# Kernel tuning notes

Measured on AMD Instinct MI355X. Metric: run time of the kernel, lower is better.

The kernel has to match this reference:

```python
import jax, jax.numpy as jnp
import numpy as np

N_NODES = 200000
N_EDGES = 6400000
N_GRAPHS = 2000


def _linear_params(key, fan_in, fan_out):
    k1, k2 = jax.random.split(key)
    bound = 1.0 / np.sqrt(fan_in)
    W = jax.random.uniform(k1, (fan_in, fan_out), minval=-bound, maxval=bound, dtype=jnp.float32)
    b = jax.random.uniform(k2, (fan_out,), minval=-bound, maxval=bound, dtype=jnp.float32)
    return W, b


def setup_inputs() -> dict:
    key = jax.random.key(0)
    ks = jax.random.split(key, 12)
    x = jax.random.normal(ks[0], (N_NODES, 2), dtype=jnp.float32)
    edge_index = jax.random.randint(ks[1], (2, N_EDGES), 0, N_NODES, dtype=jnp.int32)
    batch = jnp.sort(jax.random.randint(ks[2], (N_NODES,), 0, N_GRAPHS, dtype=jnp.int32))
    W1a, b1a = _linear_params(ks[3], 2, 16)
    W1b, b1b = _linear_params(ks[4], 16, 16)
    W2a, b2a = _linear_params(ks[5], 16, 16)
    W2b, b2b = _linear_params(ks[6], 16, 16)
    W3a, b3a = _linear_params(ks[7], 16, 16)
    W3b, b3b = _linear_params(ks[8], 16, 16)
    Wl1, bl1 = _linear_params(ks[9], 16, 16)
    Wl2, bl2 = _linear_params(ks[10], 16, 1)
    return dict(x=x, edge_index=edge_index, batch=batch,
                W1a=W1a, b1a=b1a, W1b=W1b, b1b=b1b,
                W2a=W2a, b2a=b2a, W2b=W2b, b2b=b2b,
                W3a=W3a, b3a=b3a, W3b=W3b, b3b=b3b,
                Wl1=Wl1, bl1=bl1, Wl2=Wl2, bl2=bl2)


def _gin_conv(x, src, dst, Wa, ba, Wb, bb):
    # sum-aggregate neighbor features at destination nodes; eps = 0
    msgs = x[src]                                            # [E, d]
    aggr = jax.ops.segment_sum(msgs, dst, num_segments=N_NODES)  # [N, d]
    h = x + aggr
    h = jax.nn.relu(h @ Wa + ba)
    return h @ Wb + bb


def reference(x, edge_index, batch,
              W1a, b1a, W1b, b1b,
              W2a, b2a, W2b, b2b,
              W3a, b3a, W3b, b3b,
              Wl1, bl1, Wl2, bl2):
    src, dst = edge_index[0], edge_index[1]
    h = jax.nn.relu(_gin_conv(x, src, dst, W1a, b1a, W1b, b1b))
    h = jax.nn.relu(_gin_conv(h, src, dst, W2a, b2a, W2b, b2b))
    h = jax.nn.relu(_gin_conv(h, src, dst, W3a, b3a, W3b, b3b))
    g = jax.ops.segment_sum(h, batch, num_segments=N_GRAPHS)  # global_add_pool -> [G, 16]
    g = jax.nn.relu(g @ Wl1 + bl1)
    return g @ Wl2 + bl2                                      # [G, 1]
```

## Files before the change

### kernel.cpp

```cpp
#include <hip/hip_runtime.h>

#define N_NODES 200000
#define N_EDGES 6400000
#define N_GRAPHS 2000

#define MBSHIFT 11
#define NMB 98
#define MBCAP 67584
#define CHUNK 8192
#define PBLK 782
#define PB 9

#define FSHIFT 7
#define NBUCK 1563
#define CAPF 4608

__device__ __forceinline__ float bf_lo(unsigned v) { return __uint_as_float(v << 16); }
__device__ __forceinline__ float bf_hi(unsigned v) { return __uint_as_float(v & 0xFFFF0000u); }
__device__ __forceinline__ unsigned pack_bf2(float lo, float hi) {
  unsigned a = __float_as_uint(lo), b = __float_as_uint(hi);
  a = (a + 0x7FFFu + ((a >> 16) & 1u)) >> 16;
  b = (b + 0x7FFFu + ((b >> 16) & 1u)) >> 16;
  return a | (b << 16);
}

__global__ __launch_bounds__(256) void init_cursors(int* __restrict__ gcurA,
                                                    int* __restrict__ gcur2) {
  int i = blockIdx.x * 256 + threadIdx.x;
  if (i < NMB) gcurA[i] = i * MBCAP;
  if (i < NMB * 16) gcur2[i] = i * CAPF;
}

__global__ __launch_bounds__(256) void partA(
    const int* __restrict__ src, const int* __restrict__ dst,
    int* __restrict__ gcurA, int* __restrict__ colA) {
  __shared__ int hist[NMB], base[NMB], lcur[NMB], excl[NMB];
  __shared__ int sc[128];
  __shared__ int sorted[CHUNK];
  int t = threadIdx.x;
  for (int i = t; i < NMB; i += 256) hist[i] = 0;
  __syncthreads();
  int e0 = blockIdx.x * CHUNK;
  int cnt = N_EDGES - e0; if (cnt > CHUNK) cnt = CHUNK;
  for (int i = t; i < cnt; i += 256) atomicAdd(&hist[dst[e0 + i] >> MBSHIFT], 1);
  __syncthreads();
  if (t < 128) sc[t] = (t < NMB) ? hist[t] : 0;
  __syncthreads();
  for (int off = 1; off < 128; off <<= 1) {
    int v = (t < 128 && t >= off) ? sc[t - off] : 0;
    __syncthreads();
    if (t < 128) sc[t] += v;
    __syncthreads();
  }
  if (t < NMB) {
    int e = sc[t] - hist[t];
    excl[t] = e; lcur[t] = e;
    base[t] = hist[t] ? atomicAdd(&gcurA[t], hist[t]) : 0;
  }
  __syncthreads();
  for (int i = t; i < cnt; i += 256) {
    int d = dst[e0 + i];
    int b = d >> MBSHIFT;
    int r = atomicAdd(&lcur[b], 1);
    sorted[r] = (src[e0 + i] << MBSHIFT) | (d & 2047);
  }
  __syncthreads();
  for (int b = 0; b < NMB; b++) {
    int c = hist[b], gb = base[b], lb = excl[b];
    int lim = (b + 1) * MBCAP;
    for (int i = t; i < c; i += 256) {
      int pos = gb + i;
      if (pos < lim) colA[pos] = sorted[lb + i];
    }
  }
}

__global__ __launch_bounds__(256) void partB(
    const int* __restrict__ gcurA, const int* __restrict__ colA,
    int* __restrict__ gcur2, int* __restrict__ col) {
  __shared__ int hist[16], base[16], lcur[16], excl[16];
  __shared__ int sorted[CHUNK];
  int t = threadIdx.x;
  int mb = blockIdx.x / PB, j = blockIdx.x % PB;
  int mbbase = mb * MBCAP;
  int mbcnt = gcurA[mb] - mbbase; if (mbcnt > MBCAP) mbcnt = MBCAP;
  int c0 = j * CHUNK;
  int cnt = mbcnt - c0;
  if (cnt > CHUNK) cnt = CHUNK;
  if (cnt < 0) cnt = 0;
  if (t < 16) hist[t] = 0;
  __syncthreads();
  const int* seg = colA + mbbase + c0;
  for (int i = t; i < cnt; i += 256) atomicAdd(&hist[(seg[i] & 2047) >> FSHIFT], 1);
  __syncthreads();
  if (t == 0) {
    int run = 0;
    for (int b = 0; b < 16; b++) { excl[b] = run; lcur[b] = run; run += hist[b]; }
  }
  if (t < 16) base[t] = hist[t] ? atomicAdd(&gcur2[mb * 16 + t], hist[t]) : 0;
  __syncthreads();
  for (int i = t; i < cnt; i += 256) {
    int p = seg[i];
    int b = (p & 2047) >> FSHIFT;
    int r = atomicAdd(&lcur[b], 1);
    sorted[r] = ((p >> MBSHIFT) << FSHIFT) | (p & 127);
  }
  __syncthreads();
  for (int b = 0; b < 16; b++) {
    int c = hist[b], gb = base[b], lb = excl[b];
    int lim = (mb * 16 + b + 1) * CAPF;
    for (int i = t; i < c; i += 256) {
      int pos = gb + i;
      if (pos < lim) col[pos] = sorted[lb + i];
    }
  }
}

__global__ __launch_bounds__(256) void sort_fine(
    const int* __restrict__ gcur2, int* __restrict__ col,
    int* __restrict__ rowstart, int* __restrict__ rowcnt) {
  __shared__ int hist[128], sc[128], lcur[128];
  __shared__ int sorted[CAPF];
  int t = threadIdx.x;
  int fb = blockIdx.x;
  int beg = fb * CAPF;
  int cnt = gcur2[fb] - beg; if (cnt > CAPF) cnt = CAPF;
  if (t < 128) hist[t] = 0;
  __syncthreads();
  for (int i = t; i < cnt; i += 256) atomicAdd(&hist[col[beg + i] & 127], 1);
  __syncthreads();
  if (t < 128) sc[t] = hist[t];
  __syncthreads();
  for (int off = 1; off < 128; off <<= 1) {
    int v = (t < 128 && t >= off) ? sc[t - off] : 0;
    __syncthreads();
    if (t < 128) sc[t] += v;
    __syncthreads();
  }
  if (t < 128) {
    int excl = sc[t] - hist[t];
    lcur[t] = excl;
    int n = fb * 128 + t;
    if (n < N_NODES) { rowstart[n] = beg + excl; rowcnt[n] = hist[t]; }
  }
  __syncthreads();
  for (int i = t; i < cnt; i += 256) {
    int p = col[beg + i];
    int r = atomicAdd(&lcur[p & 127], 1);
    sorted[r] = p >> FSHIFT;
  }
  __syncthreads();
  for (int i = t; i < cnt; i += 256) col[beg + i] = sorted[i];
}

__global__ __launch_bounds__(256) void aggr2_wave(
    const int* __restrict__ rowstart, const int* __restrict__ rowcnt,
    const int* __restrict__ col, const float* __restrict__ x,
    float* __restrict__ agg) {
  int n = blockIdx.x * 4 + (threadIdx.x >> 6);
  int lane = threadIdx.x & 63;
  int e0 = rowstart[n], c = rowcnt[n];
  float a0 = 0.f, a1 = 0.f;
  for (int basei = 0; basei < c; basei += 64) {
    int idx = basei + lane;
    if (idx < c) {
      int s = col[e0 + idx];
      float2 u = *reinterpret_cast<const float2*>(x + 2 * s);
      a0 += u.x; a1 += u.y;
    }
  }
#pragma unroll
  for (int off = 1; off <= 32; off <<= 1) {
    a0 += __shfl_xor(a0, off, 64);
    a1 += __shfl_xor(a1, off, 64);
  }
  if (lane == 0) {
    *reinterpret_cast<float2*>(agg + 2 * n) = make_float2(a0, a1);
  }
}

__global__ __launch_bounds__(256) void aggr16_wave(
    const int* __restrict__ rowstart, const int* __restrict__ rowcnt,
    const int* __restrict__ col, const uint4* __restrict__ hbf,
    float* __restrict__ agg) {
  int n = blockIdx.x * 4 + (threadIdx.x >> 6);
  int lane = threadIdx.x & 63;
  int e0 = rowstart[n], c = rowcnt[n];
  float a[8];
#pragma unroll
  for (int j = 0; j < 8; j++) a[j] = 0.f;
  int half = lane & 1;
  for (int basei = 0; basei < c; basei += 32) {
    int idx = basei + (lane >> 1);
    if (idx < c) {
      int s = col[e0 + idx];
      uint4 u = hbf[2 * s + half];
      a[0] += bf_lo(u.x); a[1] += bf_hi(u.x);
      a[2] += bf_lo(u.y); a[3] += bf_hi(u.y);
      a[4] += bf_lo(u.z); a[5] += bf_hi(u.z);
      a[6] += bf_lo(u.w); a[7] += bf_hi(u.w);
    }
  }
#pragma unroll
  for (int off = 2; off <= 32; off <<= 1) {
#pragma unroll
    for (int j = 0; j < 8; j++) a[j] += __shfl_xor(a[j], off, 64);
  }
  if (lane < 2) {
    float* dstp = agg + n * 16 + 8 * lane;
    *reinterpret_cast<float4*>(dstp) = make_float4(a[0], a[1], a[2], a[3]);
    *reinterpret_cast<float4*>(dstp + 4) = make_float4(a[4], a[5], a[6], a[7]);
  }
}

__global__ __launch_bounds__(256) void node_l1(
    const float* __restrict__ x, const float* __restrict__ aggr,
    const float* __restrict__ Wa, const float* __restrict__ ba,
    const float* __restrict__ Wb, const float* __restrict__ bb,
    uint4* __restrict__ out) {
  __shared__ float sWa[32], sba[16], sWb[256], sbb[16];
  int t = threadIdx.x;
  if (t < 32) sWa[t] = Wa[t];
  if (t < 16) { sba[t] = ba[t]; sbb[t] = bb[t]; }
  for (int i = t; i < 256; i += 256) sWb[i] = Wb[i];
  __syncthreads();
  int n = blockIdx.x * blockDim.x + t;
  if (n >= N_NODES) return;
  float2 xv = *reinterpret_cast<const float2*>(x + 2 * n);
  float2 av = *reinterpret_cast<const float2*>(aggr + 2 * n);
  float v0 = xv.x + av.x, v1 = xv.y + av.y;
  float h1[16];
#pragma unroll
  for (int j = 0; j < 16; j++)
    h1[j] = fmaxf(fmaf(v0, sWa[j], fmaf(v1, sWa[16 + j], sba[j])), 0.f);
  float o[16];
#pragma unroll
  for (int j = 0; j < 16; j++) {
    float s = sbb[j];
#pragma unroll
    for (int k = 0; k < 16; k++) s = fmaf(h1[k], sWb[k * 16 + j], s);
    o[j] = fmaxf(s, 0.f);
  }
  out[2 * n]     = make_uint4(pack_bf2(o[0], o[1]),  pack_bf2(o[2], o[3]),
                              pack_bf2(o[4], o[5]),  pack_bf2(o[6], o[7]));
  out[2 * n + 1] = make_uint4(pack_bf2(o[8], o[9]),  pack_bf2(o[10], o[11]),
                              pack_bf2(o[12], o[13]), pack_bf2(o[14], o[15]));
}

__global__ __launch_bounds__(256) void node16(
    const uint4* __restrict__ hin, const float* __restrict__ aggr,
    const float* __restrict__ Wa, const float* __restrict__ ba,
    const float* __restrict__ Wb, const float* __restrict__ bb,
    uint4* __restrict__ out) {
  __shared__ float sWa[256], sba[16], sWb[256], sbb[16];
  int t = threadIdx.x;
  if (t < 16) { sba[t] = ba[t]; sbb[t] = bb[t]; }
  for (int i = t; i < 256; i += 256) { sWa[i] = Wa[i]; sWb[i] = Wb[i]; }
  __syncthreads();
  int n = blockIdx.x * blockDim.x + t;
  if (n >= N_NODES) return;
  uint4 r0 = hin[2 * n], r1 = hin[2 * n + 1];
  const float4* ap = reinterpret_cast<const float4*>(aggr + 16 * n);
  float4 a0 = ap[0], a1 = ap[1], a2 = ap[2], a3 = ap[3];
  float v[16];
  v[0]  = bf_lo(r0.x) + a0.x;  v[1]  = bf_hi(r0.x) + a0.y;
  v[2]  = bf_lo(r0.y) + a0.z;  v[3]  = bf_hi(r0.y) + a0.w;
  v[4]  = bf_lo(r0.z) + a1.x;  v[5]  = bf_hi(r0.z) + a1.y;
  v[6]  = bf_lo(r0.w) + a1.z;  v[7]  = bf_hi(r0.w) + a1.w;
  v[8]  = bf_lo(r1.x) + a2.x;  v[9]  = bf_hi(r1.x) + a2.y;
  v[10] = bf_lo(r1.y) + a2.z;  v[11] = bf_hi(r1.y) + a2.w;
  v[12] = bf_lo(r1.z) + a3.x;  v[13] = bf_hi(r1.z) + a3.y;
  v[14] = bf_lo(r1.w) + a3.z;  v[15] = bf_hi(r1.w) + a3.w;
  float h1[16];
#pragma unroll
  for (int j = 0; j < 16; j++) {
    float s = sba[j];
#pragma unroll
    for (int k = 0; k < 16; k++) s = fmaf(v[k], sWa[k * 16 + j], s);
    h1[j] = fmaxf(s, 0.f);
  }
  float o[16];
#pragma unroll
  for (int j = 0; j < 16; j++) {
    float s = sbb[j];
#pragma unroll
    for (int k = 0; k < 16; k++) s = fmaf(h1[k], sWb[k * 16 + j], s);
    o[j] = fmaxf(s, 0.f);
  }
  out[2 * n]     = make_uint4(pack_bf2(o[0], o[1]),  pack_bf2(o[2], o[3]),
                              pack_bf2(o[4], o[5]),  pack_bf2(o[6], o[7]));
  out[2 * n + 1] = make_uint4(pack_bf2(o[8], o[9]),  pack_bf2(o[10], o[11]),
                              pack_bf2(o[12], o[13]), pack_bf2(o[14], o[15]));
}

__global__ __launch_bounds__(64) void pool_kernel(
    const uint4* __restrict__ h, const int* __restrict__ batch,
    float* __restrict__ g) {
  int gr = blockIdx.x;
  int lo = 0, hi = N_NODES;
  while (lo < hi) { int mid = (lo + hi) >> 1; if (batch[mid] < gr) lo = mid + 1; else hi = mid; }
  int start = lo;
  hi = N_NODES;
  while (lo < hi) { int mid = (lo + hi) >> 1; if (batch[mid] < gr + 1) lo = mid + 1; else hi = mid; }
  int end = lo;
  float acc[16];
#pragma unroll
  for (int j = 0; j < 16; j++) acc[j] = 0.f;
  for (int n = start + threadIdx.x; n < end; n += 64) {
    uint4 r0 = h[2 * n], r1 = h[2 * n + 1];
    acc[0]  += bf_lo(r0.x); acc[1]  += bf_hi(r0.x);
    acc[2]  += bf_lo(r0.y); acc[3]  += bf_hi(r0.y);
    acc[4]  += bf_lo(r0.z); acc[5]  += bf_hi(r0.z);
    acc[6]  += bf_lo(r0.w); acc[7]  += bf_hi(r0.w);
    acc[8]  += bf_lo(r1.x); acc[9]  += bf_hi(r1.x);
    acc[10] += bf_lo(r1.y); acc[11] += bf_hi(r1.y);
    acc[12] += bf_lo(r1.z); acc[13] += bf_hi(r1.z);
    acc[14] += bf_lo(r1.w); acc[15] += bf_hi(r1.w);
  }
#pragma unroll
  for (int j = 0; j < 16; j++) {
#pragma unroll
    for (int off = 32; off > 0; off >>= 1) acc[j] += __shfl_xor(acc[j], off, 64);
  }
  if (threadIdx.x == 0) {
    float4* gp = reinterpret_cast<float4*>(g + gr * 16);
#pragma unroll
    for (int q = 0; q < 4; q++)
      gp[q] = make_float4(acc[4 * q], acc[4 * q + 1], acc[4 * q + 2], acc[4 * q + 3]);
  }
}

__global__ __launch_bounds__(256) void head_kernel(
    const float* __restrict__ g,
    const float* __restrict__ Wl1, const float* __restrict__ bl1,
    const float* __restrict__ Wl2, const float* __restrict__ bl2,
    float* __restrict__ out) {
  __shared__ float sW1[256], sb1[16], sW2[16];
  int t = threadIdx.x;
  if (t < 16) { sb1[t] = bl1[t]; sW2[t] = Wl2[t]; }
  for (int i = t; i < 256; i += 256) sW1[i] = Wl1[i];
  __syncthreads();
  int gr = blockIdx.x * blockDim.x + t;
  if (gr >= N_GRAPHS) return;
  float v[16];
  const float4* gp = reinterpret_cast<const float4*>(g + 16 * gr);
#pragma unroll
  for (int q = 0; q < 4; q++) {
    float4 gv = gp[q];
    v[4 * q + 0] = gv.x; v[4 * q + 1] = gv.y; v[4 * q + 2] = gv.z; v[4 * q + 3] = gv.w;
  }
  float o = bl2[0];
#pragma unroll
  for (int j = 0; j < 16; j++) {
    float s = sb1[j];
#pragma unroll
    for (int k = 0; k < 16; k++) s = fmaf(v[k], sW1[k * 16 + j], s);
    o = fmaf(fmaxf(s, 0.f), sW2[j], o);
  }
  out[gr] = o;
}

extern "C" void kernel_launch(void* const* d_in, const int* in_sizes, int n_in,
                              void* d_out, int out_size, void* d_ws, size_t ws_size,
                              hipStream_t stream) {
  const float* x     = (const float*)d_in[0];
  const int*   ei    = (const int*)d_in[1];
  const int*   src   = ei;
  const int*   dst   = ei + N_EDGES;
  const int*   batch = (const int*)d_in[2];
  const float* W1a = (const float*)d_in[3];  const float* b1a = (const float*)d_in[4];
  const float* W1b = (const float*)d_in[5];  const float* b1b = (const float*)d_in[6];
  const float* W2a = (const float*)d_in[7];  const float* b2a = (const float*)d_in[8];
  const float* W2b = (const float*)d_in[9];  const float* b2b = (const float*)d_in[10];
  const float* W3a = (const float*)d_in[11]; const float* b3a = (const float*)d_in[12];
  const float* W3b = (const float*)d_in[13]; const float* b3b = (const float*)d_in[14];
  const float* Wl1 = (const float*)d_in[15]; const float* bl1 = (const float*)d_in[16];
  const float* Wl2 = (const float*)d_in[17]; const float* bl2 = (const float*)d_in[18];
  float* out = (float*)d_out;

  int*   gcurA    = (int*)d_ws;
  int*   gcur2    = gcurA + 128;
  int*   rowstart = gcur2 + 2048;
  int*   rowcnt   = rowstart + 200192;
  int*   col      = rowcnt + 200192;
  int*   U        = col + (size_t)NBUCK * CAPF;
  int*   colA     = U;
  float* agg      = (float*)U;
  uint4* hA       = (uint4*)(agg + (size_t)N_NODES * 16);
  uint4* hB       = hA + (size_t)N_NODES * 2;
  float* g        = (float*)(hB + (size_t)N_NODES * 2);

  const int NWAVE_BLK = N_NODES / 4;
  dim3 ngrid((N_NODES + 255) / 256);

  init_cursors<<<(NMB * 16 + 255) / 256, 256, 0, stream>>>(gcurA, gcur2);
  partA<<<PBLK, 256, 0, stream>>>(src, dst, gcurA, colA);
  partB<<<NMB * PB, 256, 0, stream>>>(gcurA, colA, gcur2, col);
  sort_fine<<<NBUCK, 256, 0, stream>>>(gcur2, col, rowstart, rowcnt);

  aggr2_wave<<<NWAVE_BLK, 256, 0, stream>>>(rowstart, rowcnt, col, x, agg);
  node_l1<<<ngrid, 256, 0, stream>>>(x, agg, W1a, b1a, W1b, b1b, hA);
  aggr16_wave<<<NWAVE_BLK, 256, 0, stream>>>(rowstart, rowcnt, col, hA, agg);
  node16<<<ngrid, 256, 0, stream>>>(hA, agg, W2a, b2a, W2b, b2b, hB);
  aggr16_wave<<<NWAVE_BLK, 256, 0, stream>>>(rowstart, rowcnt, col, hB, agg);
  node16<<<ngrid, 256, 0, stream>>>(hB, agg, W3a, b3a, W3b, b3b, hA);

  pool_kernel<<<N_GRAPHS, 64, 0, stream>>>(hA, batch, g);
  head_kernel<<<(N_GRAPHS + 255) / 256, 256, 0, stream>>>(g, Wl1, bl1, Wl2, bl2, out);
}
```

Before: 373.9 us.

## Split edge lists by source half and aggregate in two cache-friendly passes

The fine sort now buckets each destination's edges into two segments by whether the source index is below or above half the node count, producing separate row start/count arrays. The 16-feature aggregation runs as two launches, one per source half, with the second accumulating into the first's result. This shrinks the random-gather working set of node features per pass so it fits better in L2. It costs an extra kernel launch and a read-modify-write of the aggregate buffer per layer, and the half kernel uses 32 lanes per node instead of 64.

```diff
diff --git a/kernel.cpp b/kernel.cpp
--- a/kernel.cpp
+++ b/kernel.cpp
@@ -3,6 +3,7 @@
 #define N_NODES 200000
 #define N_EDGES 6400000
 #define N_GRAPHS 2000
+#define SRC_SPLIT 100000
 
 #define MBSHIFT 11
 #define NMB 98
@@ -118,35 +119,44 @@
 
 __global__ __launch_bounds__(256) void sort_fine(
     const int* __restrict__ gcur2, int* __restrict__ col,
-    int* __restrict__ rowstart, int* __restrict__ rowcnt) {
-  __shared__ int hist[128], sc[128], lcur[128];
+    int* __restrict__ rs_lo, int* __restrict__ rc_lo,
+    int* __restrict__ rs_hi, int* __restrict__ rc_hi) {
+  __shared__ int hist[256], sc[256], lcur[256];
   __shared__ int sorted[CAPF];
   int t = threadIdx.x;
   int fb = blockIdx.x;
   int beg = fb * CAPF;
   int cnt = gcur2[fb] - beg; if (cnt > CAPF) cnt = CAPF;
-  if (t < 128) hist[t] = 0;
-  __syncthreads();
-  for (int i = t; i < cnt; i += 256) atomicAdd(&hist[col[beg + i] & 127], 1);
-  __syncthreads();
-  if (t < 128) sc[t] = hist[t];
-  __syncthreads();
-  for (int off = 1; off < 128; off <<= 1) {
-    int v = (t < 128 && t >= off) ? sc[t - off] : 0;
-    __syncthreads();
-    if (t < 128) sc[t] += v;
-    __syncthreads();
-  }
-  if (t < 128) {
-    int excl = sc[t] - hist[t];
-    lcur[t] = excl;
-    int n = fb * 128 + t;
-    if (n < N_NODES) { rowstart[n] = beg + excl; rowcnt[n] = hist[t]; }
-  }
+  hist[t] = 0;
   __syncthreads();
   for (int i = t; i < cnt; i += 256) {
     int p = col[beg + i];
-    int r = atomicAdd(&lcur[p & 127], 1);
+    int key = (p & 127) | (((p >> FSHIFT) >= SRC_SPLIT) ? 128 : 0);
+    atomicAdd(&hist[key], 1);
+  }
+  __syncthreads();
+  sc[t] = hist[t];
+  __syncthreads();
+  for (int off = 1; off < 256; off <<= 1) {
+    int v = (t >= off) ? sc[t - off] : 0;
+    __syncthreads();
+    sc[t] += v;
+    __syncthreads();
+  }
+  int excl = sc[t] - hist[t];
+  lcur[t] = excl;
+  {
+    int n = fb * 128 + (t & 127);
+    if (n < N_NODES) {
+      if (t < 128) { rs_lo[n] = beg + excl; rc_lo[n] = hist[t]; }
+      else         { rs_hi[n] = beg + excl; rc_hi[n] = hist[t]; }
+    }
+  }
+  __syncthreads();
+  for (int i = t; i < cnt; i += 256) {
+    int p = col[beg + i];
+    int key = (p & 127) | (((p >> FSHIFT) >= SRC_SPLIT) ? 128 : 0);
+    int r = atomicAdd(&lcur[key], 1);
     sorted[r] = p >> FSHIFT;
   }
   __syncthreads();
@@ -154,19 +164,24 @@
 }
 
 __global__ __launch_bounds__(256) void aggr2_wave(
-    const int* __restrict__ rowstart, const int* __restrict__ rowcnt,
+    const int* __restrict__ rs_lo, const int* __restrict__ rc_lo,
+    const int* __restrict__ rs_hi, const int* __restrict__ rc_hi,
     const int* __restrict__ col, const float* __restrict__ x,
     float* __restrict__ agg) {
   int n = blockIdx.x * 4 + (threadIdx.x >> 6);
   int lane = threadIdx.x & 63;
-  int e0 = rowstart[n], c = rowcnt[n];
   float a0 = 0.f, a1 = 0.f;
-  for (int basei = 0; basei < c; basei += 64) {
-    int idx = basei + lane;
-    if (idx < c) {
-      int s = col[e0 + idx];
-      float2 u = *reinterpret_cast<const float2*>(x + 2 * s);
-      a0 += u.x; a1 += u.y;
+#pragma unroll
+  for (int seg = 0; seg < 2; seg++) {
+    int e0 = seg ? rs_hi[n] : rs_lo[n];
+    int c  = seg ? rc_hi[n] : rc_lo[n];
+    for (int basei = 0; basei < c; basei += 64) {
+      int idx = basei + lane;
+      if (idx < c) {
+        int s = col[e0 + idx];
+        float2 u = *reinterpret_cast<const float2*>(x + 2 * s);
+        a0 += u.x; a1 += u.y;
+      }
     }
   }
 #pragma unroll
@@ -179,19 +194,21 @@
   }
 }
 
-__global__ __launch_bounds__(256) void aggr16_wave(
-    const int* __restrict__ rowstart, const int* __restrict__ rowcnt,
+__global__ __launch_bounds__(256) void aggr16_half(
+    const int* __restrict__ rs, const int* __restrict__ rc,
     const int* __restrict__ col, const uint4* __restrict__ hbf,
-    float* __restrict__ agg) {
-  int n = blockIdx.x * 4 + (threadIdx.x >> 6);
+    float* __restrict__ agg, int accumulate) {
+  int w = threadIdx.x >> 6;
   int lane = threadIdx.x & 63;
-  int e0 = rowstart[n], c = rowcnt[n];
+  int l5 = lane & 31;
+  int n = blockIdx.x * 8 + w * 2 + (lane >> 5);
+  int e0 = rs[n], c = rc[n];
   float a[8];
 #pragma unroll
   for (int j = 0; j < 8; j++) a[j] = 0.f;
-  int half = lane & 1;
-  for (int basei = 0; basei < c; basei += 32) {
-    int idx = basei + (lane >> 1);
+  int half = l5 & 1;
+  for (int basei = 0; basei < c; basei += 16) {
+    int idx = basei + (l5 >> 1);
     if (idx < c) {
       int s = col[e0 + idx];
       uint4 u = hbf[2 * s + half];
@@ -202,13 +219,19 @@
     }
   }
 #pragma unroll
-  for (int off = 2; off <= 32; off <<= 1) {
+  for (int off = 2; off <= 16; off <<= 1) {
 #pragma unroll
     for (int j = 0; j < 8; j++) a[j] += __shfl_xor(a[j], off, 64);
   }
-  if (lane < 2) {
-    float* dstp = agg + n * 16 + 8 * lane;
-    *reinterpret_cast<float4*>(dstp) = make_float4(a[0], a[1], a[2], a[3]);
+  if (l5 < 2) {
+    float* dstp = agg + (size_t)n * 16 + 8 * l5;
+    if (accumulate) {
+      float4 o0 = *reinterpret_cast<float4*>(dstp);
+      float4 o1 = *reinterpret_cast<float4*>(dstp + 4);
+      a[0] += o0.x; a[1] += o0.y; a[2] += o0.z; a[3] += o0.w;
+      a[4] += o1.x; a[5] += o1.y; a[6] += o1.z; a[7] += o1.w;
+    }
+    *reinterpret_cast<float4*>(dstp)     = make_float4(a[0], a[1], a[2], a[3]);
     *reinterpret_cast<float4*>(dstp + 4) = make_float4(a[4], a[5], a[6], a[7]);
   }
 }
@@ -380,9 +403,11 @@
 
   int*   gcurA    = (int*)d_ws;
   int*   gcur2    = gcurA + 128;
-  int*   rowstart = gcur2 + 2048;
-  int*   rowcnt   = rowstart + 200192;
-  int*   col      = rowcnt + 200192;
+  int*   rs_lo    = gcur2 + 2048;
+  int*   rc_lo    = rs_lo + 200192;
+  int*   rs_hi    = rc_lo + 200192;
+  int*   rc_hi    = rs_hi + 200192;
+  int*   col      = rc_hi + 200192;
   int*   U        = col + (size_t)NBUCK * CAPF;
   int*   colA     = U;
   float* agg      = (float*)U;
@@ -391,18 +416,21 @@
   float* g        = (float*)(hB + (size_t)N_NODES * 2);
 
   const int NWAVE_BLK = N_NODES / 4;
+  const int NHALF_BLK = N_NODES / 8;
   dim3 ngrid((N_NODES + 255) / 256);
 
   init_cursors<<<(NMB * 16 + 255) / 256, 256, 0, stream>>>(gcurA, gcur2);
   partA<<<PBLK, 256, 0, stream>>>(src, dst, gcurA, colA);
   partB<<<NMB * PB, 256, 0, stream>>>(gcurA, colA, gcur2, col);
-  sort_fine<<<NBUCK, 256, 0, stream>>>(gcur2, col, rowstart, rowcnt);
-
-  aggr2_wave<<<NWAVE_BLK, 256, 0, stream>>>(rowstart, rowcnt, col, x, agg);
+  sort_fine<<<NBUCK, 256, 0, stream>>>(gcur2, col, rs_lo, rc_lo, rs_hi, rc_hi);
+
+  aggr2_wave<<<NWAVE_BLK, 256, 0, stream>>>(rs_lo, rc_lo, rs_hi, rc_hi, col, x, agg);
   node_l1<<<ngrid, 256, 0, stream>>>(x, agg, W1a, b1a, W1b, b1b, hA);
-  aggr16_wave<<<NWAVE_BLK, 256, 0, stream>>>(rowstart, rowcnt, col, hA, agg);
+  aggr16_half<<<NHALF_BLK, 256, 0, stream>>>(rs_lo, rc_lo, col, hA, agg, 0);
+  aggr16_half<<<NHALF_BLK, 256, 0, stream>>>(rs_hi, rc_hi, col, hA, agg, 1);
   node16<<<ngrid, 256, 0, stream>>>(hA, agg, W2a, b2a, W2b, b2b, hB);
-  aggr16_wave<<<NWAVE_BLK, 256, 0, stream>>>(rowstart, rowcnt, col, hB, agg);
+  aggr16_half<<<NHALF_BLK, 256, 0, stream>>>(rs_lo, rc_lo, col, hB, agg, 0);
+  aggr16_half<<<NHALF_BLK, 256, 0, stream>>>(rs_hi, rc_hi, col, hB, agg, 1);
   node16<<<ngrid, 256, 0, stream>>>(hB, agg, W3a, b3a, W3b, b3b, hA);
 
   pool_kernel<<<N_GRAPHS, 64, 0, stream>>>(hA, batch, g);
```

New measurement: 394.3 us. 1.05x slower.

## Fuse layer-1 aggregation into fine sort and flatten scatter write loops

Applied to the files above, without the earlier changes.

Computes the 2-wide layer-1 neighbor sum inside sort_fine with shared-memory float atomics, which removes the separate aggr2_wave kernel and its CSR gather pass. The per-bucket scatter loops in partA and partB become one flat loop where each element finds its bucket by binary search over the prefix sums, which balances work across threads. In exchange this adds LDS atomic contention and binary-search cost per element, and float atomic ordering makes the layer-1 sums nondeterministic.

```diff
diff --git a/kernel.cpp b/kernel.cpp
--- a/kernel.cpp
+++ b/kernel.cpp
@@ -34,7 +34,7 @@
 __global__ __launch_bounds__(256) void partA(
     const int* __restrict__ src, const int* __restrict__ dst,
     int* __restrict__ gcurA, int* __restrict__ colA) {
-  __shared__ int hist[NMB], base[NMB], lcur[NMB], excl[NMB];
+  __shared__ int hist[NMB], base[NMB], lcur[NMB];
   __shared__ int sc[128];
   __shared__ int sorted[CHUNK];
   int t = threadIdx.x;
@@ -53,8 +53,7 @@
     __syncthreads();
   }
   if (t < NMB) {
-    int e = sc[t] - hist[t];
-    excl[t] = e; lcur[t] = e;
+    lcur[t] = sc[t] - hist[t];
     base[t] = hist[t] ? atomicAdd(&gcurA[t], hist[t]) : 0;
   }
   __syncthreads();
@@ -65,20 +64,19 @@
     sorted[r] = (src[e0 + i] << MBSHIFT) | (d & 2047);
   }
   __syncthreads();
-  for (int b = 0; b < NMB; b++) {
-    int c = hist[b], gb = base[b], lb = excl[b];
-    int lim = (b + 1) * MBCAP;
-    for (int i = t; i < c; i += 256) {
-      int pos = gb + i;
-      if (pos < lim) colA[pos] = sorted[lb + i];
-    }
+  for (int i = t; i < cnt; i += 256) {
+    int lo = 0, hi = NMB;
+    while (lo < hi) { int mid = (lo + hi) >> 1; if (sc[mid] <= i) lo = mid + 1; else hi = mid; }
+    int b = lo;
+    int pos = base[b] + (i - (sc[b] - hist[b]));
+    if (pos < (b + 1) * MBCAP) colA[pos] = sorted[i];
   }
 }
 
 __global__ __launch_bounds__(256) void partB(
     const int* __restrict__ gcurA, const int* __restrict__ colA,
     int* __restrict__ gcur2, int* __restrict__ col) {
-  __shared__ int hist[16], base[16], lcur[16], excl[16];
+  __shared__ int hist[16], base[16], lcur[16], excl[16], sc16[16];
   __shared__ int sorted[CHUNK];
   int t = threadIdx.x;
   int mb = blockIdx.x / PB, j = blockIdx.x % PB;
@@ -95,7 +93,7 @@
   __syncthreads();
   if (t == 0) {
     int run = 0;
-    for (int b = 0; b < 16; b++) { excl[b] = run; lcur[b] = run; run += hist[b]; }
+    for (int b = 0; b < 16; b++) { excl[b] = run; lcur[b] = run; run += hist[b]; sc16[b] = run; }
   }
   if (t < 16) base[t] = hist[t] ? atomicAdd(&gcur2[mb * 16 + t], hist[t]) : 0;
   __syncthreads();
@@ -106,28 +104,38 @@
     sorted[r] = ((p >> MBSHIFT) << FSHIFT) | (p & 127);
   }
   __syncthreads();
-  for (int b = 0; b < 16; b++) {
-    int c = hist[b], gb = base[b], lb = excl[b];
-    int lim = (mb * 16 + b + 1) * CAPF;
-    for (int i = t; i < c; i += 256) {
-      int pos = gb + i;
-      if (pos < lim) col[pos] = sorted[lb + i];
-    }
+  for (int i = t; i < cnt; i += 256) {
+    int lo = 0, hi = 16;
+    while (lo < hi) { int mid = (lo + hi) >> 1; if (sc16[mid] <= i) lo = mid + 1; else hi = mid; }
+    int b = lo;
+    int pos = base[b] + (i - excl[b]);
+    if (pos < (mb * 16 + b + 1) * CAPF) col[pos] = sorted[i];
   }
 }
 
 __global__ __launch_bounds__(256) void sort_fine(
     const int* __restrict__ gcur2, int* __restrict__ col,
-    int* __restrict__ rowstart, int* __restrict__ rowcnt) {
+    const float* __restrict__ x,
+    int* __restrict__ rowstart, int* __restrict__ rowcnt,
+    float* __restrict__ agg2) {
   __shared__ int hist[128], sc[128], lcur[128];
+  __shared__ float sagg[256];
   __shared__ int sorted[CAPF];
   int t = threadIdx.x;
   int fb = blockIdx.x;
   int beg = fb * CAPF;
   int cnt = gcur2[fb] - beg; if (cnt > CAPF) cnt = CAPF;
   if (t < 128) hist[t] = 0;
-  __syncthreads();
-  for (int i = t; i < cnt; i += 256) atomicAdd(&hist[col[beg + i] & 127], 1);
+  sagg[t] = 0.f;
+  __syncthreads();
+  for (int i = t; i < cnt; i += 256) {
+    int p = col[beg + i];
+    int s = p >> FSHIFT, d = p & 127;
+    atomicAdd(&hist[d], 1);
+    float2 u = *reinterpret_cast<const float2*>(x + 2 * s);
+    atomicAdd(&sagg[d * 2 + 0], u.x);
+    atomicAdd(&sagg[d * 2 + 1], u.y);
+  }
   __syncthreads();
   if (t < 128) sc[t] = hist[t];
   __syncthreads();
@@ -143,6 +151,10 @@
     int n = fb * 128 + t;
     if (n < N_NODES) { rowstart[n] = beg + excl; rowcnt[n] = hist[t]; }
   }
+  {
+    int n2 = fb * 256 + t;
+    if (n2 < N_NODES * 2) agg2[n2] = sagg[t];
+  }
   __syncthreads();
   for (int i = t; i < cnt; i += 256) {
     int p = col[beg + i];
@@ -151,32 +163,6 @@
   }
   __syncthreads();
   for (int i = t; i < cnt; i += 256) col[beg + i] = sorted[i];
-}
-
-__global__ __launch_bounds__(256) void aggr2_wave(
-    const int* __restrict__ rowstart, const int* __restrict__ rowcnt,
-    const int* __restrict__ col, const float* __restrict__ x,
-    float* __restrict__ agg) {
-  int n = blockIdx.x * 4 + (threadIdx.x >> 6);
-  int lane = threadIdx.x & 63;
-  int e0 = rowstart[n], c = rowcnt[n];
-  float a0 = 0.f, a1 = 0.f;
-  for (int basei = 0; basei < c; basei += 64) {
-    int idx = basei + lane;
-    if (idx < c) {
-      int s = col[e0 + idx];
-      float2 u = *reinterpret_cast<const float2*>(x + 2 * s);
-      a0 += u.x; a1 += u.y;
-    }
-  }
-#pragma unroll
-  for (int off = 1; off <= 32; off <<= 1) {
-    a0 += __shfl_xor(a0, off, 64);
-    a1 += __shfl_xor(a1, off, 64);
-  }
-  if (lane == 0) {
-    *reinterpret_cast<float2*>(agg + 2 * n) = make_float2(a0, a1);
-  }
 }
 
 __global__ __launch_bounds__(256) void aggr16_wave(
@@ -207,14 +193,14 @@
     for (int j = 0; j < 8; j++) a[j] += __shfl_xor(a[j], off, 64);
   }
   if (lane < 2) {
-    float* dstp = agg + n * 16 + 8 * lane;
-    *reinterpret_cast<float4*>(dstp) = make_float4(a[0], a[1], a[2], a[3]);
+    float* dstp = agg + (size_t)n * 16 + 8 * lane;
+    *reinterpret_cast<float4*>(dstp)     = make_float4(a[0], a[1], a[2], a[3]);
     *reinterpret_cast<float4*>(dstp + 4) = make_float4(a[4], a[5], a[6], a[7]);
   }
 }
 
 __global__ __launch_bounds__(256) void node_l1(
-    const float* __restrict__ x, const float* __restrict__ aggr,
+    const float* __restrict__ x, const float* __restrict__ agg2,
     const float* __restrict__ Wa, const float* __restrict__ ba,
     const float* __restrict__ Wb, const float* __restrict__ bb,
     uint4* __restrict__ out) {
@@ -227,7 +213,7 @@
   int n = blockIdx.x * blockDim.x + t;
   if (n >= N_NODES) return;
   float2 xv = *reinterpret_cast<const float2*>(x + 2 * n);
-  float2 av = *reinterpret_cast<const float2*>(aggr + 2 * n);
+  float2 av = *reinterpret_cast<const float2*>(agg2 + 2 * n);
   float v0 = xv.x + av.x, v1 = xv.y + av.y;
   float h1[16];
 #pragma unroll
@@ -382,7 +368,8 @@
   int*   gcur2    = gcurA + 128;
   int*   rowstart = gcur2 + 2048;
   int*   rowcnt   = rowstart + 200192;
-  int*   col      = rowcnt + 200192;
+  float* agg2     = (float*)(rowcnt + 200192);
+  int*   col      = (int*)agg2 + 400384;
   int*   U        = col + (size_t)NBUCK * CAPF;
   int*   colA     = U;
   float* agg      = (float*)U;
@@ -396,10 +383,9 @@
   init_cursors<<<(NMB * 16 + 255) / 256, 256, 0, stream>>>(gcurA, gcur2);
   partA<<<PBLK, 256, 0, stream>>>(src, dst, gcurA, colA);
   partB<<<NMB * PB, 256, 0, stream>>>(gcurA, colA, gcur2, col);
-  sort_fine<<<NBUCK, 256, 0, stream>>>(gcur2, col, rowstart, rowcnt);
-
-  aggr2_wave<<<NWAVE_BLK, 256, 0, stream>>>(rowstart, rowcnt, col, x, agg);
-  node_l1<<<ngrid, 256, 0, stream>>>(x, agg, W1a, b1a, W1b, b1b, hA);
+  sort_fine<<<NBUCK, 256, 0, stream>>>(gcur2, col, x, rowstart, rowcnt, agg2);
+
+  node_l1<<<ngrid, 256, 0, stream>>>(x, agg2, W1a, b1a, W1b, b1b, hA);
   aggr16_wave<<<NWAVE_BLK, 256, 0, stream>>>(rowstart, rowcnt, col, hA, agg);
   node16<<<ngrid, 256, 0, stream>>>(hA, agg, W2a, b2a, W2b, b2b, hB);
   aggr16_wave<<<NWAVE_BLK, 256, 0, stream>>>(rowstart, rowcnt, col, hB, agg);
```

Result: slower. 404.7 us (+8.2%).
